# Optimization experiments

Hardware: AMD Instinct MI355X
Metric: run time of the kernel (lower is better)

Reference implementation:

```python
import jax, jax.numpy as jnp
import numpy as np

NUM_CAMS = 1
NUM_HEADS = 1
NUM_LEVELS = 1
NUM_POINTS = 4
NUM_DEPTH = 128
EMBED = 128  # must equal NUM_DEPTH (output_proj is applied to the depth axis)


def setup_inputs() -> dict:
    key0 = jax.random.key(0)
    ks = jax.random.split(key0, 12)
    bsv, nq, nv = 1, 1024, 1024  # nq == nv == H*W (32*32)
    off_dim = NUM_CAMS * NUM_HEADS * NUM_LEVELS * NUM_DEPTH * NUM_POINTS * 2  # 1024
    aw_dim = NUM_CAMS * NUM_HEADS * NUM_LEVELS * NUM_DEPTH * NUM_POINTS       # 512
    return {
        "query": jax.random.normal(ks[0], (bsv, nq, EMBED), jnp.float32),
        "key": jax.random.normal(ks[1], (NUM_CAMS, nv, bsv, EMBED), jnp.float32),
        "value": jax.random.normal(ks[2], (NUM_CAMS, nv, bsv, EMBED), jnp.float32),
        "ref_3d": jax.random.uniform(ks[3], (bsv * NUM_CAMS, nq * NUM_DEPTH, 2), jnp.float32),
        "spatial_shapes": jnp.array([[32, 32]], dtype=jnp.int32),
        "W_off": jax.random.normal(ks[4], (EMBED, off_dim), jnp.float32) * 0.02,
        "b_off": jax.random.normal(ks[5], (off_dim,), jnp.float32) * 0.02,
        "W_attn": jax.random.normal(ks[6], (EMBED, aw_dim), jnp.float32) * 0.02,
        "b_attn": jax.random.normal(ks[7], (aw_dim,), jnp.float32) * 0.02,
        "W_v": jax.random.normal(ks[8], (EMBED, EMBED), jnp.float32) / np.sqrt(EMBED),
        "b_v": jnp.zeros((EMBED,), jnp.float32),
        "W_o": jax.random.normal(ks[9], (EMBED, EMBED), jnp.float32) / np.sqrt(EMBED),
        "b_o": jnp.zeros((EMBED,), jnp.float32),
    }


def _bilinear_sample(val, H, W, x, y):
    """grid_sample(align_corners=False, padding=zeros) equivalent.
    val: [B, H*W, D]; x, y: [B, Q, P] in pixel coords. Returns [B, Q, P, D]."""
    B, Q, P = x.shape
    D = val.shape[-1]
    x0f = jnp.floor(x); y0f = jnp.floor(y)
    ix0 = x0f.astype(jnp.int32); iy0 = y0f.astype(jnp.int32)
    wx1 = x - x0f; wy1 = y - y0f
    wx0 = 1.0 - wx1; wy0 = 1.0 - wy1

    def corner(ix, iy, w):
        valid = (ix >= 0) & (ix < W) & (iy >= 0) & (iy < H)
        idx = jnp.clip(iy, 0, H - 1) * W + jnp.clip(ix, 0, W - 1)  # [B,Q,P]
        g = jnp.take_along_axis(val, idx.reshape(B, Q * P)[:, :, None], axis=1)
        g = g.reshape(B, Q, P, D)
        return g * (w * valid.astype(val.dtype))[..., None]

    return (corner(ix0, iy0, wx0 * wy0)
            + corner(ix0 + 1, iy0, wx1 * wy0)
            + corner(ix0, iy0 + 1, wx0 * wy1)
            + corner(ix0 + 1, iy0 + 1, wx1 * wy1))


def reference(query, key, value, ref_3d, spatial_shapes,
              W_off, b_off, W_attn, b_attn, W_v, b_v, W_o, b_o):
    bsv, nq, E = query.shape
    cams, nv, bs, _ = key.shape
    identity = query

    # key/value: [cams, nv, bs, E] -> [bsv, nv, E]
    key2 = jnp.transpose(key, (2, 0, 1, 3)).reshape(bsv, nv, E)
    val = jnp.flip(value, axis=0)
    val = jnp.transpose(val, (2, 0, 1, 3)).reshape(bsv, nv, E)
    val = val @ W_v + b_v
    val = val.reshape(bsv * cams, nv, E)  # num_heads=1 -> head_dim=E

    # offsets / attention weights (heads=levels=1 axes squeezed)
    off = (query @ W_off + b_off).reshape(bsv, nq, cams, NUM_DEPTH, NUM_POINTS, 2)
    aw = (query @ W_attn + b_attn).reshape(bsv, nq, cams, NUM_DEPTH, NUM_LEVELS * NUM_POINTS)
    aw = jax.nn.softmax(aw, axis=-1).reshape(bsv, nq, cams, NUM_DEPTH, NUM_POINTS)
    off = jnp.transpose(off, (0, 2, 1, 3, 4, 5)).reshape(bsv * cams, nq * NUM_DEPTH, NUM_POINTS, 2)
    aw = jnp.transpose(aw, (0, 2, 1, 3, 4)).reshape(bsv * cams, nq * NUM_DEPTH, NUM_POINTS)

    H = spatial_shapes[0, 0]
    W = spatial_shapes[0, 1]
    norm = jnp.stack([W, H]).astype(off.dtype)  # [W, H]
    loc = ref_3d[:, :, None, :] + off / norm    # [B, Qe, P, 2] in [0,1]
    x = loc[..., 0] * W.astype(loc.dtype) - 0.5
    y = loc[..., 1] * H.astype(loc.dtype) - 0.5

    sampled = _bilinear_sample(val, H, W, x, y)          # [B, Qe, P, E]
    out = jnp.einsum('bqpe,bqp->bqe', sampled, aw)       # weighted sum over points

    out = out.reshape(bsv, cams, nq, NUM_DEPTH, E).mean(axis=1)  # [bsv, nq, depth, E]
    out = (out * key2[:, :, None, :]).mean(axis=-1)              # [bsv, nq, depth]
    out = out @ W_o + b_o                                        # depth == EMBED
    return out + identity  # dropout = identity in eval
```

## Files before the change

### kernel.cpp

```cpp
#include <hip/hip_runtime.h>
#include <hip/hip_bf16.h>


#define NQ   1024
#define NV   1024
#define ND   128
#define NP   4
#define IMG_W 32
#define IMG_H 32

__device__ __forceinline__ void gemm_tile64(
    const float* __restrict__ A,
    const float* __restrict__ B,
    int N, bool nt,
    const float* __restrict__ bias,
    const float* __restrict__ cvec,
    float* __restrict__ C,
    int m0, int n0, float* sA, float* sB) {
  const int tid = threadIdx.x;

#pragma unroll
  for (int k = 0; k < 8; ++k) {
    int c = tid + k * 256;
    int m = c & 63, e4 = c >> 6;
    const float4 v = *(const float4*)(A + (size_t)(m0 + m) * 128 + e4 * 4);
    sA[(e4 * 4 + 0) * 64 + m] = v.x;
    sA[(e4 * 4 + 1) * 64 + m] = v.y;
    sA[(e4 * 4 + 2) * 64 + m] = v.z;
    sA[(e4 * 4 + 3) * 64 + m] = v.w;
  }
  if (nt) {
#pragma unroll
    for (int k = 0; k < 8; ++k) {
      int c = tid + k * 256;
      int n = c & 63, e4 = c >> 6;
      const float4 v = *(const float4*)(B + (size_t)(n0 + n) * 128 + e4 * 4);
      sB[(e4 * 4 + 0) * 64 + n] = v.x;
      sB[(e4 * 4 + 1) * 64 + n] = v.y;
      sB[(e4 * 4 + 2) * 64 + n] = v.z;
      sB[(e4 * 4 + 3) * 64 + n] = v.w;
    }
  } else {
#pragma unroll
    for (int k = 0; k < 8; ++k) {
      int c = tid + k * 256;
      int n4 = c & 15, e = c >> 4;
      *(float4*)(sB + e * 64 + n4 * 4) =
          *(const float4*)(B + (size_t)e * N + n0 + n4 * 4);
    }
  }
  __syncthreads();

  const int tx = tid & 15, ty = tid >> 4;
  float acc[4][4] = {};
#pragma unroll 8
  for (int e = 0; e < 128; ++e) {
    const float4 a = *(const float4*)(sA + e * 64 + ty * 4);
    const float4 b = *(const float4*)(sB + e * 64 + tx * 4);
    acc[0][0] += a.x * b.x; acc[0][1] += a.x * b.y; acc[0][2] += a.x * b.z; acc[0][3] += a.x * b.w;
    acc[1][0] += a.y * b.x; acc[1][1] += a.y * b.y; acc[1][2] += a.y * b.z; acc[1][3] += a.y * b.w;
    acc[2][0] += a.z * b.x; acc[2][1] += a.z * b.y; acc[2][2] += a.z * b.z; acc[2][3] += a.z * b.w;
    acc[3][0] += a.w * b.x; acc[3][1] += a.w * b.y; acc[3][2] += a.w * b.z; acc[3][3] += a.w * b.w;
  }

  float4 bv = make_float4(0.f, 0.f, 0.f, 0.f);
  if (bias) bv = *(const float4*)(bias + n0 + tx * 4);
#pragma unroll
  for (int i = 0; i < 4; ++i) {
    const int m = m0 + ty * 4 + i;
    float cv = cvec ? cvec[m] : 0.f;
    float4 r;
    r.x = acc[i][0] + bv.x + cv;
    r.y = acc[i][1] + bv.y + cv;
    r.z = acc[i][2] + bv.z + cv;
    r.w = acc[i][3] + bv.w + cv;
    *(float4*)(C + (size_t)m * N + n0 + tx * 4) = r;
  }
}

__global__ __launch_bounds__(256, 2) void p1_kernel(
    const float* __restrict__ query, const float* __restrict__ key,
    const float* __restrict__ W_off, const float* __restrict__ b_off,
    const float* __restrict__ W_attn, const float* __restrict__ b_attn,
    const float* __restrict__ W_v, const float* __restrict__ b_v,
    float* __restrict__ off_ws, float* __restrict__ aw_ws,
    float* __restrict__ keyp_ws, float* __restrict__ c_ws) {
  __shared__ float sA[128 * 64];
  __shared__ float sB[128 * 64];
  const int t = blockIdx.x;
  if (t < 256) {
    gemm_tile64(query, W_off, 1024, false, b_off, nullptr, off_ws,
                (t >> 4) * 64, (t & 15) * 64, sA, sB);
  } else if (t < 384) {
    const int u = t - 256;
    gemm_tile64(query, W_attn, 512, false, b_attn, nullptr, aw_ws,
                (u >> 3) * 64, (u & 7) * 64, sA, sB);
  } else if (t < 416) {
    const int u = t - 384;
    gemm_tile64(key, W_v, 128, true, nullptr, nullptr, keyp_ws,
                (u >> 1) * 64, (u & 1) * 64, sA, sB);
  } else {
    for (int i = 0; i < 4; ++i) {
      const int q = threadIdx.x + i * 256;
      float s = 0.f;
      for (int e = 0; e < 128; ++e) s += key[(size_t)q * 128 + e] * b_v[e];
      c_ws[q] = s;
    }
  }
}

__global__ __launch_bounds__(256, 2) void p2_kernel(
    const float* __restrict__ keyp_ws, const float* __restrict__ value,
    const float* __restrict__ c_ws, float* __restrict__ dotv_ws) {
  __shared__ float sA[128 * 64];
  __shared__ float sB[128 * 64];
  const int t = blockIdx.x;
  gemm_tile64(keyp_ws, value, 1024, true, nullptr, c_ws, dotv_ws,
              (t >> 4) * 64, (t & 15) * 64, sA, sB);
}

__global__ __launch_bounds__(256) void p3_kernel(
    const float* __restrict__ dotv,
    const float* __restrict__ off,
    const float* __restrict__ awr,
    const float* __restrict__ ref3d,
    const float* __restrict__ query,
    const float* __restrict__ W_o,
    const float* __restrict__ b_o,
    float* __restrict__ out) {
  __shared__ float img[2][NV];
  __shared__ float o1s[2][ND];

  const int tid = threadIdx.x;
  const int q0 = blockIdx.x * 2;

#pragma unroll
  for (int k = 0; k < 2; ++k) {
    int c = tid + k * 256;
    int qq = c >> 8, v4 = c & 255;
    *(float4*)(&img[qq][v4 * 4]) =
        *(const float4*)(dotv + (size_t)(q0 + qq) * NV + v4 * 4);
  }
  __syncthreads();

  {
    const int qq = tid >> 7;
    const int q = q0 + qq;
    const int d = tid & 127;
    const float* im = img[qq];
    const size_t qe = (size_t)q * ND + d;

    const float rx = ref3d[qe * 2 + 0];
    const float ry = ref3d[qe * 2 + 1];

    const float* awp = awr + (size_t)q * (ND * NP) + d * NP;
    const float a0 = awp[0], a1 = awp[1], a2 = awp[2], a3 = awp[3];
    const float mx = fmaxf(fmaxf(a0, a1), fmaxf(a2, a3));
    const float e0 = __expf(a0 - mx), e1 = __expf(a1 - mx),
                e2 = __expf(a2 - mx), e3 = __expf(a3 - mx);
    const float inv = 1.0f / (e0 + e1 + e2 + e3);
    const float w[4] = {e0 * inv, e1 * inv, e2 * inv, e3 * inv};

    const float* op = off + (size_t)q * (ND * NP * 2) + d * (NP * 2);

    float acc = 0.0f;
#pragma unroll
    for (int p = 0; p < NP; ++p) {
      const float x = rx * (float)IMG_W + op[p * 2 + 0] - 0.5f;
      const float y = ry * (float)IMG_H + op[p * 2 + 1] - 0.5f;
      const float xf = floorf(x), yf = floorf(y);
      const int ix0 = (int)xf, iy0 = (int)yf;
      const float wx1 = x - xf, wy1 = y - yf;
      const float wx0 = 1.0f - wx1, wy0 = 1.0f - wy1;

      float s = 0.0f;
#pragma unroll
      for (int cy = 0; cy < 2; ++cy) {
#pragma unroll
        for (int cx = 0; cx < 2; ++cx) {
          const int ix = ix0 + cx, iy = iy0 + cy;
          const bool valid = (ix >= 0) & (ix < IMG_W) & (iy >= 0) & (iy < IMG_H);
          const int cix = min(max(ix, 0), IMG_W - 1);
          const int ciy = min(max(iy, 0), IMG_H - 1);
          const float wgt = (cx ? wx1 : wx0) * (cy ? wy1 : wy0);
          s += valid ? im[ciy * IMG_W + cix] * wgt : 0.0f;
        }
      }
      acc += w[p] * s;
    }
    o1s[qq][d] = acc * (1.0f / 128.0f);
  }
  __syncthreads();

  {
    const int qq = tid >> 7;
    const int q = q0 + qq;
    const int n = tid & 127;
    float acc = b_o[n] + query[(size_t)q * 128 + n];
#pragma unroll 8
    for (int d = 0; d < 128; ++d)
      acc += o1s[qq][d] * W_o[(size_t)d * 128 + n];
    out[(size_t)q * 128 + n] = acc;
  }
}

extern "C" void kernel_launch(void* const* d_in, const int* in_sizes, int n_in,
                              void* d_out, int out_size, void* d_ws, size_t ws_size,
                              hipStream_t stream) {
  const float* query  = (const float*)d_in[0];
  const float* key    = (const float*)d_in[1];
  const float* value  = (const float*)d_in[2];
  const float* ref3d  = (const float*)d_in[3];
  const float* W_off  = (const float*)d_in[5];
  const float* b_off  = (const float*)d_in[6];
  const float* W_attn = (const float*)d_in[7];
  const float* b_attn = (const float*)d_in[8];
  const float* W_v    = (const float*)d_in[9];
  const float* b_v    = (const float*)d_in[10];
  const float* W_o    = (const float*)d_in[11];
  const float* b_o    = (const float*)d_in[12];
  float* out = (float*)d_out;

  float* ws = (float*)d_ws;
  float* off_ws  = ws;
  float* aw_ws   = off_ws + (size_t)NQ * 1024;
  float* keyp_ws = aw_ws + (size_t)NQ * 512;
  float* c_ws    = keyp_ws + (size_t)NQ * 128;
  float* dotv_ws = c_ws + 1024;

  p1_kernel<<<417, 256, 0, stream>>>(query, key, W_off, b_off, W_attn, b_attn,
                                     W_v, b_v, off_ws, aw_ws, keyp_ws, c_ws);
  p2_kernel<<<256, 256, 0, stream>>>(keyp_ws, value, c_ws, dotv_ws);
  p3_kernel<<<512, 256, 0, stream>>>(dotv_ws, off_ws, aw_ws, ref3d, query,
                                     W_o, b_o, out);
}
```

Before: 114.1 us.

## Fuse three phases into one cooperative kernel with grid syncs

```diff
diff --git a/kernel.cpp b/kernel.cpp
--- a/kernel.cpp
+++ b/kernel.cpp
@@ -1,5 +1,8 @@
 #include <hip/hip_runtime.h>
 #include <hip/hip_bf16.h>
+#include <hip/hip_cooperative_groups.h>
+
+namespace cg = cooperative_groups;
 
 
 #define NQ   1024
@@ -9,14 +12,17 @@
 #define IMG_W 32
 #define IMG_H 32
 
+struct KArgs {
+  const float *query, *key, *value, *ref3d;
+  const float *W_off, *b_off, *W_attn, *b_attn, *W_v, *b_v, *W_o, *b_o;
+  float *off_ws, *aw_ws, *keyp_ws, *c_ws, *dotv_ws, *out;
+};
+
 __device__ __forceinline__ void gemm_tile64(
-    const float* __restrict__ A,
-    const float* __restrict__ B,
+    const float* __restrict__ A, const float* __restrict__ B,
     int N, bool nt,
-    const float* __restrict__ bias,
-    const float* __restrict__ cvec,
-    float* __restrict__ C,
-    int m0, int n0, float* sA, float* sB) {
+    const float* __restrict__ bias, const float* __restrict__ cvec,
+    float* __restrict__ C, int m0, int n0, float* sA, float* sB) {
   const int tid = threadIdx.x;
 
 #pragma unroll
@@ -78,67 +84,67 @@
   }
 }
 
-__global__ __launch_bounds__(256, 2) void p1_kernel(
-    const float* __restrict__ query, const float* __restrict__ key,
-    const float* __restrict__ W_off, const float* __restrict__ b_off,
-    const float* __restrict__ W_attn, const float* __restrict__ b_attn,
-    const float* __restrict__ W_v, const float* __restrict__ b_v,
-    float* __restrict__ off_ws, float* __restrict__ aw_ws,
-    float* __restrict__ keyp_ws, float* __restrict__ c_ws) {
-  __shared__ float sA[128 * 64];
-  __shared__ float sB[128 * 64];
-  const int t = blockIdx.x;
-  if (t < 256) {
-    gemm_tile64(query, W_off, 1024, false, b_off, nullptr, off_ws,
-                (t >> 4) * 64, (t & 15) * 64, sA, sB);
-  } else if (t < 384) {
-    const int u = t - 256;
-    gemm_tile64(query, W_attn, 512, false, b_attn, nullptr, aw_ws,
-                (u >> 3) * 64, (u & 7) * 64, sA, sB);
-  } else if (t < 416) {
-    const int u = t - 384;
-    gemm_tile64(key, W_v, 128, true, nullptr, nullptr, keyp_ws,
-                (u >> 1) * 64, (u & 1) * 64, sA, sB);
-  } else {
-    for (int i = 0; i < 4; ++i) {
-      const int q = threadIdx.x + i * 256;
-      float s = 0.f;
-      for (int e = 0; e < 128; ++e) s += key[(size_t)q * 128 + e] * b_v[e];
-      c_ws[q] = s;
-    }
-  }
-}
-
-__global__ __launch_bounds__(256, 2) void p2_kernel(
-    const float* __restrict__ keyp_ws, const float* __restrict__ value,
-    const float* __restrict__ c_ws, float* __restrict__ dotv_ws) {
-  __shared__ float sA[128 * 64];
-  __shared__ float sB[128 * 64];
-  const int t = blockIdx.x;
-  gemm_tile64(keyp_ws, value, 1024, true, nullptr, c_ws, dotv_ws,
-              (t >> 4) * 64, (t & 15) * 64, sA, sB);
-}
-
-__global__ __launch_bounds__(256) void p3_kernel(
-    const float* __restrict__ dotv,
-    const float* __restrict__ off,
-    const float* __restrict__ awr,
-    const float* __restrict__ ref3d,
-    const float* __restrict__ query,
-    const float* __restrict__ W_o,
-    const float* __restrict__ b_o,
-    float* __restrict__ out) {
-  __shared__ float img[2][NV];
-  __shared__ float o1s[2][ND];
-
+__device__ __forceinline__ void dotv_tile32x64(
+    const float* __restrict__ keyp, const float* __restrict__ value,
+    const float* __restrict__ cvec, float* __restrict__ dotv,
+    int m0, int n0, float* sKA, float* sVB) {
   const int tid = threadIdx.x;
-  const int q0 = blockIdx.x * 2;
-
+#pragma unroll
+  for (int k = 0; k < 4; ++k) {
+    int c = tid + k * 256;
+    int m = c & 31, e4 = c >> 5;
+    const float4 v = *(const float4*)(keyp + (size_t)(m0 + m) * 128 + e4 * 4);
+    sKA[(e4 * 4 + 0) * 32 + m] = v.x;
+    sKA[(e4 * 4 + 1) * 32 + m] = v.y;
+    sKA[(e4 * 4 + 2) * 32 + m] = v.z;
+    sKA[(e4 * 4 + 3) * 32 + m] = v.w;
+  }
+#pragma unroll
+  for (int k = 0; k < 8; ++k) {
+    int c = tid + k * 256;
+    int n = c & 63, e4 = c >> 6;
+    const float4 v = *(const float4*)(value + (size_t)(n0 + n) * 128 + e4 * 4);
+    sVB[(e4 * 4 + 0) * 64 + n] = v.x;
+    sVB[(e4 * 4 + 1) * 64 + n] = v.y;
+    sVB[(e4 * 4 + 2) * 64 + n] = v.z;
+    sVB[(e4 * 4 + 3) * 64 + n] = v.w;
+  }
+  __syncthreads();
+
+  const int tx = tid & 15, ty = tid >> 4;
+  float acc[2][4] = {};
+#pragma unroll 8
+  for (int e = 0; e < 128; ++e) {
+    const float2 av = *(const float2*)(sKA + e * 32 + ty * 2);
+    const float4 bv = *(const float4*)(sVB + e * 64 + tx * 4);
+    acc[0][0] += av.x * bv.x; acc[0][1] += av.x * bv.y;
+    acc[0][2] += av.x * bv.z; acc[0][3] += av.x * bv.w;
+    acc[1][0] += av.y * bv.x; acc[1][1] += av.y * bv.y;
+    acc[1][2] += av.y * bv.z; acc[1][3] += av.y * bv.w;
+  }
+#pragma unroll
+  for (int i = 0; i < 2; ++i) {
+    const int m = m0 + ty * 2 + i;
+    const float cv = cvec[m];
+    float4 r;
+    r.x = acc[i][0] + cv; r.y = acc[i][1] + cv;
+    r.z = acc[i][2] + cv; r.w = acc[i][3] + cv;
+    *(float4*)(dotv + (size_t)m * NV + n0 + tx * 4) = r;
+  }
+}
+
+__device__ __forceinline__ void sample_and_out(
+    const float* __restrict__ dotv, const float* __restrict__ off,
+    const float* __restrict__ awr, const float* __restrict__ ref3d,
+    const float* __restrict__ query, const float* __restrict__ W_o,
+    const float* __restrict__ b_o, float* __restrict__ out,
+    int q0, float* img , float* o1s ) {
+  const int tid = threadIdx.x;
 #pragma unroll
   for (int k = 0; k < 2; ++k) {
     int c = tid + k * 256;
     int qq = c >> 8, v4 = c & 255;
-    *(float4*)(&img[qq][v4 * 4]) =
+    *(float4*)(&img[qq * NV + v4 * 4]) =
         *(const float4*)(dotv + (size_t)(q0 + qq) * NV + v4 * 4);
   }
   __syncthreads();
@@ -147,7 +153,7 @@
     const int qq = tid >> 7;
     const int q = q0 + qq;
     const int d = tid & 127;
-    const float* im = img[qq];
+    const float* im = img + qq * NV;
     const size_t qe = (size_t)q * ND + d;
 
     const float rx = ref3d[qe * 2 + 0];
@@ -188,7 +194,7 @@
       }
       acc += w[p] * s;
     }
-    o1s[qq][d] = acc * (1.0f / 128.0f);
+    o1s[qq * ND + d] = acc * (1.0f / 128.0f);
   }
   __syncthreads();
 
@@ -197,40 +203,130 @@
     const int q = q0 + qq;
     const int n = tid & 127;
     float acc = b_o[n] + query[(size_t)q * 128 + n];
+    const float* o1 = o1s + qq * ND;
 #pragma unroll 8
     for (int d = 0; d < 128; ++d)
-      acc += o1s[qq][d] * W_o[(size_t)d * 128 + n];
+      acc += o1[d] * W_o[(size_t)d * 128 + n];
     out[(size_t)q * 128 + n] = acc;
   }
+}
+
+__global__ __launch_bounds__(256, 2) void fused_all(KArgs a) {
+  cg::grid_group grid = cg::this_grid();
+  __shared__ float smem[16384];
+  const int b = blockIdx.x;
+  const int tid = threadIdx.x;
+
+  {
+    float* sA = smem;
+    float* sB = smem + 8192;
+    if (b < 256) {
+      gemm_tile64(a.query, a.W_off, 1024, false, a.b_off, nullptr, a.off_ws,
+                  (b >> 4) * 64, (b & 15) * 64, sA, sB);
+    } else if (b < 384) {
+      const int u = b - 256;
+      gemm_tile64(a.query, a.W_attn, 512, false, a.b_attn, nullptr, a.aw_ws,
+                  (u >> 3) * 64, (u & 7) * 64, sA, sB);
+    } else if (b < 416) {
+      const int u = b - 384;
+      gemm_tile64(a.key, a.W_v, 128, true, nullptr, nullptr, a.keyp_ws,
+                  (u >> 1) * 64, (u & 1) * 64, sA, sB);
+    } else if (b == 416) {
+      for (int i = 0; i < 4; ++i) {
+        const int q = tid + i * 256;
+        float s = 0.f;
+        for (int e = 0; e < 128; ++e) s += a.key[(size_t)q * 128 + e] * a.b_v[e];
+        a.c_ws[q] = s;
+      }
+    }
+  }
+  grid.sync();
+
+  {
+    float* sKA = smem;
+    float* sVB = smem + 4096;
+    const int m0 = (b & 31) * 32;
+    const int n0 = (b >> 5) * 64;
+    dotv_tile32x64(a.keyp_ws, a.value, a.c_ws, a.dotv_ws, m0, n0, sKA, sVB);
+  }
+  grid.sync();
+
+  {
+    float* img = smem;
+    float* o1s = smem + 2048;
+    sample_and_out(a.dotv_ws, a.off_ws, a.aw_ws, a.ref3d, a.query,
+                   a.W_o, a.b_o, a.out, b * 2, img, o1s);
+  }
+}
+
+__global__ __launch_bounds__(256, 2) void p1_kernel(KArgs a) {
+  __shared__ float smem[16384];
+  float* sA = smem; float* sB = smem + 8192;
+  const int t = blockIdx.x;
+  if (t < 256) {
+    gemm_tile64(a.query, a.W_off, 1024, false, a.b_off, nullptr, a.off_ws,
+                (t >> 4) * 64, (t & 15) * 64, sA, sB);
+  } else if (t < 384) {
+    const int u = t - 256;
+    gemm_tile64(a.query, a.W_attn, 512, false, a.b_attn, nullptr, a.aw_ws,
+                (u >> 3) * 64, (u & 7) * 64, sA, sB);
+  } else if (t < 416) {
+    const int u = t - 384;
+    gemm_tile64(a.key, a.W_v, 128, true, nullptr, nullptr, a.keyp_ws,
+                (u >> 1) * 64, (u & 1) * 64, sA, sB);
+  } else {
+    for (int i = 0; i < 4; ++i) {
+      const int q = threadIdx.x + i * 256;
+      float s = 0.f;
+      for (int e = 0; e < 128; ++e) s += a.key[(size_t)q * 128 + e] * a.b_v[e];
+      a.c_ws[q] = s;
+    }
+  }
+}
+
+__global__ __launch_bounds__(256, 2) void p2_kernel(KArgs a) {
+  __shared__ float smem[12288];
+  const int b = blockIdx.x;
+  dotv_tile32x64(a.keyp_ws, a.value, a.c_ws, a.dotv_ws,
+                 (b & 31) * 32, (b >> 5) * 64, smem, smem + 4096);
+}
+
+__global__ __launch_bounds__(256) void p3_kernel(KArgs a) {
+  __shared__ float smem[2304];
+  sample_and_out(a.dotv_ws, a.off_ws, a.aw_ws, a.ref3d, a.query,
+                 a.W_o, a.b_o, a.out, blockIdx.x * 2, smem, smem + 2048);
 }
 
 extern "C" void kernel_launch(void* const* d_in, const int* in_sizes, int n_in,
                               void* d_out, int out_size, void* d_ws, size_t ws_size,
                               hipStream_t stream) {
-  const float* query  = (const float*)d_in[0];
-  const float* key    = (const float*)d_in[1];
-  const float* value  = (const float*)d_in[2];
-  const float* ref3d  = (const float*)d_in[3];
-  const float* W_off  = (const float*)d_in[5];
-  const float* b_off  = (const float*)d_in[6];
-  const float* W_attn = (const float*)d_in[7];
-  const float* b_attn = (const float*)d_in[8];
-  const float* W_v    = (const float*)d_in[9];
-  const float* b_v    = (const float*)d_in[10];
-  const float* W_o    = (const float*)d_in[11];
-  const float* b_o    = (const float*)d_in[12];
-  float* out = (float*)d_out;
-
   float* ws = (float*)d_ws;
-  float* off_ws  = ws;
-  float* aw_ws   = off_ws + (size_t)NQ * 1024;
-  float* keyp_ws = aw_ws + (size_t)NQ * 512;
-  float* c_ws    = keyp_ws + (size_t)NQ * 128;
-  float* dotv_ws = c_ws + 1024;
-
-  p1_kernel<<<417, 256, 0, stream>>>(query, key, W_off, b_off, W_attn, b_attn,
-                                     W_v, b_v, off_ws, aw_ws, keyp_ws, c_ws);
-  p2_kernel<<<256, 256, 0, stream>>>(keyp_ws, value, c_ws, dotv_ws);
-  p3_kernel<<<512, 256, 0, stream>>>(dotv_ws, off_ws, aw_ws, ref3d, query,
-                                     W_o, b_o, out);
-}
+  KArgs a;
+  a.query  = (const float*)d_in[0];
+  a.key    = (const float*)d_in[1];
+  a.value  = (const float*)d_in[2];
+  a.ref3d  = (const float*)d_in[3];
+  a.W_off  = (const float*)d_in[5];
+  a.b_off  = (const float*)d_in[6];
+  a.W_attn = (const float*)d_in[7];
+  a.b_attn = (const float*)d_in[8];
+  a.W_v    = (const float*)d_in[9];
+  a.b_v    = (const float*)d_in[10];
+  a.W_o    = (const float*)d_in[11];
+  a.b_o    = (const float*)d_in[12];
+  a.off_ws  = ws;
+  a.aw_ws   = a.off_ws + (size_t)NQ * 1024;
+  a.keyp_ws = a.aw_ws + (size_t)NQ * 512;
+  a.c_ws    = a.keyp_ws + (size_t)NQ * 128;
+  a.dotv_ws = a.c_ws + 1024;
+  a.out     = (float*)d_out;
+
+  void* kargs[] = { (void*)&a };
+  hipError_t err = hipLaunchCooperativeKernel(
+      (const void*)fused_all, dim3(512), dim3(256), kargs, 0, stream);
+  if (err != hipSuccess) {
+    p1_kernel<<<417, 256, 0, stream>>>(a);
+    p2_kernel<<<512, 256, 0, stream>>>(a);
+    p3_kernel<<<512, 256, 0, stream>>>(a);
+  }
+}
```

New measurement: 260.2 us. +128.1%, slower.
